# Performance work log

Measured on AMD Instinct MI355X. Metric: run time of the kernel, lower is better.

The kernel has to match this reference:

```python
import jax, jax.numpy as jnp
import numpy as np

B, S, D, H = 4, 2048, 1024, 16
DK = D // H

def setup_inputs() -> dict:
    key = jax.random.key(0)
    ks = jax.random.split(key, 8)
    scale = 1.0 / np.sqrt(D)
    q = jax.random.normal(ks[0], (B, S, D), dtype=jnp.float32)
    k = jax.random.normal(ks[1], (B, S, D), dtype=jnp.float32)
    v = jax.random.normal(ks[2], (B, S, D), dtype=jnp.float32)
    # Linear weights stored as [in, out] (applied as x @ W)
    W_q = jax.random.normal(ks[3], (D, D), dtype=jnp.float32) * scale
    W_k = jax.random.normal(ks[4], (D, D), dtype=jnp.float32) * scale
    W_v = jax.random.normal(ks[5], (D, D), dtype=jnp.float32) * scale
    W_o = jax.random.normal(ks[6], (D, D), dtype=jnp.float32) * scale
    mask = jnp.tril(jnp.ones((S, S), dtype=bool))[None, None]  # [1,1,S,S] causal
    return {"q": q, "k": k, "v": v, "W_q": W_q, "W_k": W_k, "W_v": W_v, "W_o": W_o, "mask": mask}

def reference(q, k, v, W_q, W_k, W_v, W_o, mask) -> jnp.ndarray:
    b, sq, _ = q.shape
    sk = k.shape[1]
    # project and split heads: [B,S,D] -> [B,H,S,dk]
    Q = (q @ W_q).reshape(b, sq, H, DK).transpose(0, 2, 1, 3)
    K = (k @ W_k).reshape(b, sk, H, DK).transpose(0, 2, 1, 3)
    V = (v @ W_v).reshape(b, sk, H, DK).transpose(0, 2, 1, 3)
    scores = jnp.einsum('bhqd,bhkd->bhqk', Q, K) / jnp.sqrt(jnp.float32(DK))
    scores = jnp.where(mask, scores, jnp.float32(-1e9))
    attn = jax.nn.softmax(scores, axis=-1)
    out = jnp.einsum('bhqk,bhkd->bhqd', attn, V)  # [B,H,Sq,dk]
    out = out.transpose(0, 2, 1, 3).reshape(b, sq, D)
    return out @ W_o
```

## Files before the change

kernel.cpp:

```cpp
#include <hip/hip_runtime.h>
#include <hip/hip_bf16.h>
#include <stdint.h>

#define B_  4
#define S_  2048
#define D_  1024
#define H_  16
#define DK_ 64
#define M_  (B_*S_)
#define MD_ ((size_t)M_*D_)

typedef unsigned short u16;
typedef unsigned int   u32;
using bh8 = __attribute__((ext_vector_type(8))) short;
using fx4 = __attribute__((ext_vector_type(4))) float;
using us4 = __attribute__((ext_vector_type(4))) unsigned short;

#define C1_ 0.18033688011112042f

__device__ __forceinline__ u16 f2bf(float f){
  union { float f; u32 u; } v; v.f = f;
  u32 r = v.u + 0x7FFFu + ((v.u >> 16) & 1u);
  return (u16)(r >> 16);
}
__device__ __forceinline__ u16 f2bf_fast(float f){
  union { float f; u32 u; } v; v.f = f;
  return (u16)((v.u + 0x8000u) >> 16);
}
__device__ __forceinline__ float fexp2(float x){
  float r;
  asm("v_exp_f32 %0, %1\n\ts_nop 0" : "=v"(r) : "v"(x));
  return r;
}
__device__ __forceinline__ void gl16(const void* g, void* l){
  __builtin_amdgcn_global_load_lds(
      (const __attribute__((address_space(1))) unsigned int*)g,
      (__attribute__((address_space(3))) unsigned int*)l, 16, 0, 0);
}

__global__ __launch_bounds__(256) void prep_k(const float* __restrict__ q,
                                              const float* __restrict__ k,
                                              const float* __restrict__ v,
                                              const float* __restrict__ W0,
                                              const float* __restrict__ W1,
                                              const float* __restrict__ W2,
                                              const float* __restrict__ W3,
                                              u16* __restrict__ dq,
                                              u16* __restrict__ dk,
                                              u16* __restrict__ dv,
                                              u16* __restrict__ WT){
  int id = blockIdx.x;
  int tid = threadIdx.x;
  if (id < 12288){
    int z = id >> 12;
    int i = (id & 4095)*256 + tid;
    const float* in = (z==0)? q : (z==1)? k : v;
    u16* out = (z==0)? dq : (z==1)? dk : dv;
    const float4* p = (const float4*)(in + (size_t)i*8);
    float4 a0 = p[0], a1 = p[1];
    u16 o[8];
    o[0]=f2bf(a0.x); o[1]=f2bf(a0.y); o[2]=f2bf(a0.z); o[3]=f2bf(a0.w);
    o[4]=f2bf(a1.x); o[5]=f2bf(a1.y); o[6]=f2bf(a1.z); o[7]=f2bf(a1.w);
    *(bh8*)(out + (size_t)i*8) = *(bh8*)o;
  } else {
    int id2 = id - 12288;
    int z = id2 >> 10, b2 = id2 & 1023;
    int bx = b2 & 31, by = b2 >> 5;
    const float* in = (z==0)? W0 : (z==1)? W1 : (z==2)? W2 : W3;
    float scale = (z==0)? C1_ : 1.0f;
    u16* o = WT + (size_t)z*1024*1024;
    __shared__ u16 tile[32][33];
    int tx = tid & 31, ty = tid >> 5;
    int x0 = bx*32, y0 = by*32;
    #pragma unroll
    for (int j=0;j<32;j+=8) tile[ty+j][tx] = f2bf(in[(size_t)(y0+ty+j)*D_ + x0+tx]*scale);
    __syncthreads();
    #pragma unroll
    for (int j=0;j<32;j+=8) o[(size_t)(x0+ty+j)*D_ + y0+tx] = tile[tx][ty+j];
  }
}

template<int MODE>
__global__ __launch_bounds__(512) void gemm8(const u16* __restrict__ Aqk,
                                             const u16* __restrict__ Av,
                                             const u16* __restrict__ WTb,
                                             u16* __restrict__ Cqk,
                                             u16* __restrict__ VtOut,
                                             float* __restrict__ Cf){
  __shared__ __align__(16) u16 AL[2][128*64];
  __shared__ __align__(16) u16 BL[2][256*64];

  int hbid = blockIdx.x;
  int xcd = hbid & 7, slot = hbid >> 3;
  int pg  = xcd * (MODE==0 ? 24 : 8) + (slot >> 2);
  int x   = slot & 3;
  int y   = (MODE==0) ? (pg & 63) : pg;
  int z   = (MODE==0) ? (pg >> 6) : 0;

  const u16* A  = (MODE==0 && z==2) ? Av : (Aqk + (size_t)z*MD_);
  const u16* BT = WTb + (size_t)z*1024*1024;
  int tid = threadIdx.x;
  int w = tid >> 6, lane = tid & 63, quad = lane >> 4, ln = lane & 15;
  int wm = w >> 2, wn = w & 3;
  int rowBase = y*128, colBase = x*256;

  auto sA = [&](int buf, int kt, int c){
    int s = c*512 + tid;
    int row = s >> 3, kc = (s & 7) ^ (row & 7);
    gl16(&A[(size_t)(rowBase + row)*D_ + kt*64 + kc*8], &AL[buf][s*8]);
  };
  auto sB = [&](int buf, int kt, int c){
    int s = c*512 + tid;
    int row = s >> 3, kc = (s & 7) ^ (row & 7);
    gl16(&BT[(size_t)(colBase + row)*D_ + kt*64 + kc*8], &BL[buf][s*8]);
  };
  auto ridx = [&](int row, int kc){ return row*64 + ((kc ^ (row & 7))*8); };

  fx4 acc[4][4];
  #pragma unroll
  for (int i=0;i<4;i++)
    #pragma unroll
    for (int j=0;j<4;j++) acc[i][j] = (fx4){0.f,0.f,0.f,0.f};

  sA(0,0,0); sA(0,0,1); sB(0,0,0); sB(0,0,1); sB(0,0,2); sB(0,0,3);
  sB(1,1,0); sB(1,1,1); sB(1,1,2);
  asm volatile("s_waitcnt vmcnt(3)" ::: "memory");
  __builtin_amdgcn_s_barrier();

  for (int it = 0; it < 8; ++it){
    int t = 2*it;
    bool h2 = (t+2 < 16), h3 = (t+3 < 16);
    #pragma unroll
    for (int half = 0; half < 2; ++half){
      const u16* Ab = &AL[half][0];
      const u16* Bb = &BL[half][0];

      bh8 bfr[4][2], af0[2][2], af1[2][2];
      #pragma unroll
      for (int n=0;n<4;n++)
        #pragma unroll
        for (int ks=0;ks<2;ks++)
          bfr[n][ks] = *(const bh8*)(&Bb[ridx(wn*64 + n*16 + ln, ks*4+quad)]);
      #pragma unroll
      for (int mi=0;mi<2;mi++)
        #pragma unroll
        for (int ks=0;ks<2;ks++)
          af0[mi][ks] = *(const bh8*)(&Ab[ridx(wm*64 + mi*16 + ln, ks*4+quad)]);
      #pragma unroll
      for (int mi=0;mi<2;mi++)
        #pragma unroll
        for (int ks=0;ks<2;ks++)
          af1[mi][ks] = *(const bh8*)(&Ab[ridx(wm*64 + 32 + mi*16 + ln, ks*4+quad)]);

      if (half == 0){
        sB(1, t+1, 3); sA(1, t+1, 0); sA(1, t+1, 1);
      } else if (h2){
        sB(0, t+2, 3); sA(0, t+2, 0); sA(0, t+2, 1);
      }
      __builtin_amdgcn_s_barrier();
      asm volatile("s_waitcnt lgkmcnt(4)" ::: "memory");
      __builtin_amdgcn_s_setprio(1);
      #pragma unroll
      for (int mi=0;mi<2;mi++)
        #pragma unroll
        for (int n=0;n<4;n++)
          #pragma unroll
          for (int ks=0;ks<2;ks++)
            acc[mi][n] = __builtin_amdgcn_mfma_f32_16x16x32_bf16(
                            af0[mi][ks], bfr[n][ks], acc[mi][n], 0,0,0);
      __builtin_amdgcn_s_setprio(0);
      __builtin_amdgcn_s_barrier();

      if (half == 0){
        if (h2){ sB(0, t+2, 0); sB(0, t+2, 1); sB(0, t+2, 2); }
        if (h2) asm volatile("s_waitcnt vmcnt(3)" ::: "memory");
        else    asm volatile("s_waitcnt vmcnt(0)" ::: "memory");
      } else {
        if (h3){ sB(1, t+3, 0); sB(1, t+3, 1); sB(1, t+3, 2); }
        if (h3) asm volatile("s_waitcnt vmcnt(3)" ::: "memory");
        else    asm volatile("s_waitcnt vmcnt(0)" ::: "memory");
      }
      __builtin_amdgcn_s_barrier();
      asm volatile("s_waitcnt lgkmcnt(0)" ::: "memory");
      __builtin_amdgcn_s_setprio(1);
      #pragma unroll
      for (int mi=0;mi<2;mi++)
        #pragma unroll
        for (int n=0;n<4;n++)
          #pragma unroll
          for (int ks=0;ks<2;ks++)
            acc[2+mi][n] = __builtin_amdgcn_mfma_f32_16x16x32_bf16(
                              af1[mi][ks], bfr[n][ks], acc[2+mi][n], 0,0,0);
      __builtin_amdgcn_s_setprio(0);
      __builtin_amdgcn_s_barrier();
    }
  }

  #pragma unroll
  for (int m=0;m<4;m++){
    int row0 = rowBase + wm*64 + m*16 + quad*4;
    #pragma unroll
    for (int n=0;n<4;n++){
      int col = colBase + wn*64 + n*16 + ln;
      if (MODE == 1){
        #pragma unroll
        for (int r=0;r<4;r++)
          Cf[(size_t)(row0 + r)*D_ + col] = acc[m][n][r];
      } else if (z == 2){
        int bb = row0 >> 11, tok = row0 & (S_-1);
        int hh = col >> 6,  vd  = col & 63;
        us4 pk;
        #pragma unroll
        for (int r=0;r<4;r++) pk[r] = f2bf(acc[m][n][r]);
        *(us4*)&VtOut[((size_t)((bb*16+hh)*64+vd))*S_ + tok] = pk;
      } else {
        #pragma unroll
        for (int r=0;r<4;r++)
          (Cqk + (size_t)z*MD_)[(size_t)(row0 + r)*D_ + col] = f2bf(acc[m][n][r]);
      }
    }
  }
}

__global__ __launch_bounds__(256) void attn_k(const u16* __restrict__ Q,
                                              const u16* __restrict__ Kp,
                                              const u16* __restrict__ VtG,
                                              u16* __restrict__ O){
  __shared__ __align__(16) u16 Kt[2][64*64];
  __shared__ __align__(16) u16 Vt[2][64*64];
  __shared__ __align__(16) u16 Pb[4*16*64];

  int bh = blockIdx.x; int b = bh>>4, h = bh&15;
  int qt = (int)gridDim.y - 1 - (int)blockIdx.y;
  int tid = threadIdx.x;
  int w = tid >> 6, lane = tid & 63, quad = lane >> 4, ln = lane & 15;
  int q0w = qt*128 + w*32;
  size_t headoff = (size_t)h*DK_;

  bh8 qf[2][2];
  #pragma unroll
  for (int rg=0; rg<2; rg++){
    const u16* qp = Q + (size_t)(b*S_ + q0w + rg*16 + ln)*D_ + headoff + quad*8;
    qf[rg][0] = *(const bh8*)qp;
    qf[rg][1] = *(const bh8*)(qp + 32);
  }

  float m_i[2], l_i[2];
  fx4 oacc[2][4];
  #pragma unroll
  for (int rg=0; rg<2; rg++){
    m_i[rg] = -3e38f; l_i[rg] = 0.f;
    #pragma unroll
    for (int r=0;r<4;r++) oacc[rg][r] = (fx4){0.f,0.f,0.f,0.f};
  }

  auto stage = [&](int k0, int bi){
    #pragma unroll
    for (int i=0;i<2;i++){
      int s = i*256 + tid;
      int n = s >> 3, kc = (s & 7) ^ (n & 7);
      gl16(&Kp[(size_t)(b*S_ + k0 + n)*D_ + headoff + kc*8], &Kt[bi][s*8]);
    }
    #pragma unroll
    for (int i=0;i<2;i++){
      int s = i*256 + tid;
      int vd = s >> 3, c = (s & 7) ^ (vd & 7);
      gl16(&VtG[(size_t)(bh*64 + vd)*S_ + k0 + c*8], &Vt[bi][s*8]);
    }
  };

  u16* Pw = &Pb[w*16*64];
  int ntiles = 2*qt + 2;

  stage(0, 0);
  __syncthreads();

  for (int kt=0; kt<ntiles; kt++){
    int cur = kt & 1;
    if (kt+1 < ntiles) stage((kt+1)*64, cur^1);
    const u16* Kc = Kt[cur];
    const u16* Vc = Vt[cur];
    int k0 = kt*64;
    bool diag = (kt >= 2*qt);

    #pragma unroll
    for (int rg=0; rg<2; rg++){
      fx4 sacc[4];
      __builtin_amdgcn_s_setprio(1);
      #pragma unroll
      for (int t=0;t<4;t++){
        int n = t*16 + ln;
        bh8 kf0 = *(const bh8*)(&Kc[(n*8 + ( quad    ^ (ln&7)))*8]);
        bh8 kf1 = *(const bh8*)(&Kc[(n*8 + ((4+quad) ^ (ln&7)))*8]);
        fx4 zz = (fx4){0.f,0.f,0.f,0.f};
        zz = __builtin_amdgcn_mfma_f32_16x16x32_bf16(kf0, qf[rg][0], zz, 0,0,0);
        zz = __builtin_amdgcn_mfma_f32_16x16x32_bf16(kf1, qf[rg][1], zz, 0,0,0);
        sacc[t] = zz;
      }
      __builtin_amdgcn_s_setprio(0);

      int qg = q0w + rg*16 + ln;
      if (diag){
        #pragma unroll
        for (int t=0;t<4;t++){
          #pragma unroll
          for (int r=0;r<4;r++){
            int kg = k0 + t*16 + quad*4 + r;
            sacc[t][r] = (kg <= qg) ? sacc[t][r] : -3e38f;
          }
        }
      }

      float tm[4];
      #pragma unroll
      for (int t=0;t<4;t++)
        tm[t] = fmaxf(fmaxf(sacc[t][0], sacc[t][1]), fmaxf(sacc[t][2], sacc[t][3]));
      float mloc = fmaxf(fmaxf(tm[0], tm[1]), fmaxf(tm[2], tm[3]));
      mloc = fmaxf(mloc, __shfl_xor(mloc, 16, 64));
      mloc = fmaxf(mloc, __shfl_xor(mloc, 32, 64));

      if (__any(mloc > m_i[rg] + 8.0f)){
        float mn = fmaxf(m_i[rg], mloc);
        float alpha = fexp2(m_i[rg] - mn);
        m_i[rg] = mn;
        l_i[rg] *= alpha;
        float al[4];
        #pragma unroll
        for (int r=0;r<4;r++) al[r] = __shfl(alpha, quad*4 + r, 64);
        #pragma unroll
        for (int vt=0;vt<4;vt++)
          #pragma unroll
          for (int r=0;r<4;r++)
            oacc[rg][vt][r] *= al[r];
      }
      float mn = m_i[rg];

      float ts[4];
      #pragma unroll
      for (int t=0;t<4;t++){
        #pragma unroll
        for (int r=0;r<4;r++) sacc[t][r] = fexp2(sacc[t][r] - mn);
        ts[t] = (sacc[t][0] + sacc[t][1]) + (sacc[t][2] + sacc[t][3]);
      }
      float rs = (ts[0] + ts[1]) + (ts[2] + ts[3]);
      rs += __shfl_xor(rs, 16, 64);
      rs += __shfl_xor(rs, 32, 64);
      l_i[rg] += rs;

      #pragma unroll
      for (int t=0;t<4;t++){
        int hs = (t*4 + quad) ^ (ln & 14);
        us4 pk;
        #pragma unroll
        for (int r=0;r<4;r++) pk[r] = f2bf_fast(sacc[t][r]);
        *(us4*)&Pw[ln*64 + hs*4] = pk;
      }
      asm volatile("s_waitcnt lgkmcnt(0)" ::: "memory");

      __builtin_amdgcn_s_setprio(1);
      #pragma unroll
      for (int s2=0; s2<2; s2++){
        int c = s2*4 + quad;
        int pm = c ^ ((ln>>1) & 7);
        bh8 pf = *(const bh8*)(&Pw[ln*64 + pm*8]);
        #pragma unroll
        for (int vt=0; vt<4; vt++){
          int vd = vt*16 + ln;
          bh8 vf = *(const bh8*)(&Vc[(vd*8 + (c ^ (ln&7)))*8]);
          oacc[rg][vt] = __builtin_amdgcn_mfma_f32_16x16x32_bf16(pf, vf, oacc[rg][vt], 0,0,0);
        }
      }
      __builtin_amdgcn_s_setprio(0);
      asm volatile("s_waitcnt lgkmcnt(0)" ::: "memory");
    }
    __syncthreads();
  }

  #pragma unroll
  for (int rg=0; rg<2; rg++){
    float linv = 1.0f / l_i[rg];
    float lb[4];
    #pragma unroll
    for (int r=0;r<4;r++) lb[r] = __shfl(linv, quad*4 + r, 64);
    #pragma unroll
    for (int r=0;r<4;r++){
      #pragma unroll
      for (int vt=0; vt<4; vt++){
        float ov = oacc[rg][vt][r] * lb[r];
        O[(size_t)(b*S_ + q0w + rg*16 + quad*4 + r)*D_ + headoff + vt*16 + ln] = f2bf(ov);
      }
    }
  }
}

extern "C" void kernel_launch(void* const* d_in, const int* in_sizes, int n_in,
                              void* d_out, int out_size, void* d_ws, size_t ws_size,
                              hipStream_t stream){
  const float* q  = (const float*)d_in[0];
  const float* k  = (const float*)d_in[1];
  const float* v  = (const float*)d_in[2];
  const float* Wq = (const float*)d_in[3];
  const float* Wk = (const float*)d_in[4];
  const float* Wv = (const float*)d_in[5];
  const float* Wo = (const float*)d_in[6];

  u16* ws  = (u16*)d_ws;
  u16* WT  = ws;
  u16* xa  = WT + (size_t)4*1024*1024;
  u16* xb  = xa + MD_;
  u16* Qp  = xb + MD_;
  u16* Kp  = Qp + MD_;

  u16* vb  = (u16*)d_out;
  u16* VtG = vb + MD_;

  prep_k<<<dim3(16384), 256, 0, stream>>>(q, k, v, Wq, Wk, Wv, Wo, xa, xb, vb, WT);

  gemm8<0><<<dim3(768), 512, 0, stream>>>(xa, vb, WT, Qp, VtG, nullptr);

  attn_k<<<dim3(B_*H_, S_/128), 256, 0, stream>>>(Qp, Kp, VtG, Qp);

  gemm8<1><<<dim3(256), 512, 0, stream>>>(Qp, nullptr, WT + (size_t)3*1024*1024,
                                          nullptr, nullptr, (float*)d_out);
}
```

Measured before the change: 326.5 us.

## Pair mirrored causal query tiles per block to balance attention work

Each attention block now handles two 64-row query tiles, j1=31-p and j2=p, back to back. This gives every block the same 33 KV tiles, replacing blocks of 128 query rows whose KV tile count grew with their position. Each wave now owns 16 query rows instead of 32, and the grid drops to 16 blocks per head on the y axis. The aim is to remove the causal load imbalance and tail effects, at the cost of each staged K/V tile feeding half as many query rows, which roughly doubles K/V staging traffic per query.

```diff
diff --git a/kernel.cpp b/kernel.cpp
--- a/kernel.cpp
+++ b/kernel.cpp
@@ -231,28 +231,40 @@
   __shared__ __align__(16) u16 Pb[4*16*64];
 
   int bh = blockIdx.x; int b = bh>>4, h = bh&15;
-  int qt = (int)gridDim.y - 1 - (int)blockIdx.y;
+  int p  = blockIdx.y;
+  int j1 = 31 - p, j2 = p;
   int tid = threadIdx.x;
   int w = tid >> 6, lane = tid & 63, quad = lane >> 4, ln = lane & 15;
-  int q0w = qt*128 + w*32;
   size_t headoff = (size_t)h*DK_;
 
-  bh8 qf[2][2];
-  #pragma unroll
-  for (int rg=0; rg<2; rg++){
-    const u16* qp = Q + (size_t)(b*S_ + q0w + rg*16 + ln)*D_ + headoff + quad*8;
-    qf[rg][0] = *(const bh8*)qp;
-    qf[rg][1] = *(const bh8*)(qp + 32);
-  }
-
-  float m_i[2], l_i[2];
-  fx4 oacc[2][4];
-  #pragma unroll
-  for (int rg=0; rg<2; rg++){
-    m_i[rg] = -3e38f; l_i[rg] = 0.f;
-    #pragma unroll
-    for (int r=0;r<4;r++) oacc[rg][r] = (fx4){0.f,0.f,0.f,0.f};
-  }
+  int q0w;
+  bh8 qf0, qf1;
+  float m_i, l_i;
+  fx4 oacc[4];
+
+  auto loadQ = [&](int j){
+    q0w = j*64 + w*16;
+    const u16* qp = Q + (size_t)(b*S_ + q0w + ln)*D_ + headoff + quad*8;
+    qf0 = *(const bh8*)qp;
+    qf1 = *(const bh8*)(qp + 32);
+    m_i = -3e38f; l_i = 0.f;
+    #pragma unroll
+    for (int r=0;r<4;r++) oacc[r] = (fx4){0.f,0.f,0.f,0.f};
+  };
+
+  auto writeO = [&](){
+    float linv = 1.0f / l_i;
+    float lb[4];
+    #pragma unroll
+    for (int r=0;r<4;r++) lb[r] = __shfl(linv, quad*4 + r, 64);
+    #pragma unroll
+    for (int r=0;r<4;r++)
+      #pragma unroll
+      for (int vt=0; vt<4; vt++){
+        float ov = oacc[vt][r] * lb[r];
+        O[(size_t)(b*S_ + q0w + quad*4 + r)*D_ + headoff + vt*16 + ln] = f2bf(ov);
+      }
+  };
 
   auto stage = [&](int k0, int bi){
     #pragma unroll
@@ -270,127 +282,116 @@
   };
 
   u16* Pw = &Pb[w*16*64];
-  int ntiles = 2*qt + 2;
-
+  const int nt = 33;
+  auto k0_of = [&](int i){ return (i <= j1) ? i*64 : (i - j1 - 1)*64; };
+
+  loadQ(j1);
   stage(0, 0);
   __syncthreads();
 
-  for (int kt=0; kt<ntiles; kt++){
-    int cur = kt & 1;
-    if (kt+1 < ntiles) stage((kt+1)*64, cur^1);
+  for (int i=0; i<nt; i++){
+    int cur = i & 1;
+    if (i+1 < nt) stage(k0_of(i+1), cur^1);
     const u16* Kc = Kt[cur];
     const u16* Vc = Vt[cur];
-    int k0 = kt*64;
-    bool diag = (kt >= 2*qt);
-
-    #pragma unroll
-    for (int rg=0; rg<2; rg++){
-      fx4 sacc[4];
-      __builtin_amdgcn_s_setprio(1);
-      #pragma unroll
-      for (int t=0;t<4;t++){
-        int n = t*16 + ln;
-        bh8 kf0 = *(const bh8*)(&Kc[(n*8 + ( quad    ^ (ln&7)))*8]);
-        bh8 kf1 = *(const bh8*)(&Kc[(n*8 + ((4+quad) ^ (ln&7)))*8]);
-        fx4 zz = (fx4){0.f,0.f,0.f,0.f};
-        zz = __builtin_amdgcn_mfma_f32_16x16x32_bf16(kf0, qf[rg][0], zz, 0,0,0);
-        zz = __builtin_amdgcn_mfma_f32_16x16x32_bf16(kf1, qf[rg][1], zz, 0,0,0);
-        sacc[t] = zz;
+    int k0 = k0_of(i);
+    bool diag = (i == j1) || (i == nt-1);
+
+    fx4 sacc[4];
+    __builtin_amdgcn_s_setprio(1);
+    #pragma unroll
+    for (int t=0;t<4;t++){
+      int n = t*16 + ln;
+      bh8 kf0 = *(const bh8*)(&Kc[(n*8 + ( quad    ^ (ln&7)))*8]);
+      bh8 kf1 = *(const bh8*)(&Kc[(n*8 + ((4+quad) ^ (ln&7)))*8]);
+      fx4 zz = (fx4){0.f,0.f,0.f,0.f};
+      zz = __builtin_amdgcn_mfma_f32_16x16x32_bf16(kf0, qf0, zz, 0,0,0);
+      zz = __builtin_amdgcn_mfma_f32_16x16x32_bf16(kf1, qf1, zz, 0,0,0);
+      sacc[t] = zz;
+    }
+    __builtin_amdgcn_s_setprio(0);
+
+    int qg = q0w + ln;
+    if (diag){
+      #pragma unroll
+      for (int t=0;t<4;t++)
+        #pragma unroll
+        for (int r=0;r<4;r++){
+          int kg = k0 + t*16 + quad*4 + r;
+          sacc[t][r] = (kg <= qg) ? sacc[t][r] : -3e38f;
+        }
+    }
+
+    float tm[4];
+    #pragma unroll
+    for (int t=0;t<4;t++)
+      tm[t] = fmaxf(fmaxf(sacc[t][0], sacc[t][1]), fmaxf(sacc[t][2], sacc[t][3]));
+    float mloc = fmaxf(fmaxf(tm[0], tm[1]), fmaxf(tm[2], tm[3]));
+    mloc = fmaxf(mloc, __shfl_xor(mloc, 16, 64));
+    mloc = fmaxf(mloc, __shfl_xor(mloc, 32, 64));
+
+    if (__any(mloc > m_i + 8.0f)){
+      float mn = fmaxf(m_i, mloc);
+      float alpha = fexp2(m_i - mn);
+      m_i = mn;
+      l_i *= alpha;
+      float al[4];
+      #pragma unroll
+      for (int r=0;r<4;r++) al[r] = __shfl(alpha, quad*4 + r, 64);
+      #pragma unroll
+      for (int vt=0;vt<4;vt++)
+        #pragma unroll
+        for (int r=0;r<4;r++)
+          oacc[vt][r] *= al[r];
+    }
+    float mn = m_i;
+
+    float ts[4];
+    #pragma unroll
+    for (int t=0;t<4;t++){
+      #pragma unroll
+      for (int r=0;r<4;r++) sacc[t][r] = fexp2(sacc[t][r] - mn);
+      ts[t] = (sacc[t][0] + sacc[t][1]) + (sacc[t][2] + sacc[t][3]);
+    }
+    float rs = (ts[0] + ts[1]) + (ts[2] + ts[3]);
+    rs += __shfl_xor(rs, 16, 64);
+    rs += __shfl_xor(rs, 32, 64);
+    l_i += rs;
+
+    #pragma unroll
+    for (int t=0;t<4;t++){
+      int hs = (t*4 + quad) ^ (ln & 14);
+      us4 pk;
+      #pragma unroll
+      for (int r=0;r<4;r++) pk[r] = f2bf_fast(sacc[t][r]);
+      *(us4*)&Pw[ln*64 + hs*4] = pk;
+    }
+    asm volatile("s_waitcnt lgkmcnt(0)" ::: "memory");
+
+    __builtin_amdgcn_s_setprio(1);
+    #pragma unroll
+    for (int s2=0; s2<2; s2++){
+      int c = s2*4 + quad;
+      int pm = c ^ ((ln>>1) & 7);
+      bh8 pf = *(const bh8*)(&Pw[ln*64 + pm*8]);
+      #pragma unroll
+      for (int vt=0; vt<4; vt++){
+        int vd = vt*16 + ln;
+        bh8 vf = *(const bh8*)(&Vc[(vd*8 + (c ^ (ln&7)))*8]);
+        oacc[vt] = __builtin_amdgcn_mfma_f32_16x16x32_bf16(pf, vf, oacc[vt], 0,0,0);
       }
-      __builtin_amdgcn_s_setprio(0);
-
-      int qg = q0w + rg*16 + ln;
-      if (diag){
-        #pragma unroll
-        for (int t=0;t<4;t++){
-          #pragma unroll
-          for (int r=0;r<4;r++){
-            int kg = k0 + t*16 + quad*4 + r;
-            sacc[t][r] = (kg <= qg) ? sacc[t][r] : -3e38f;
-          }
-        }
-      }
-
-      float tm[4];
-      #pragma unroll
-      for (int t=0;t<4;t++)
-        tm[t] = fmaxf(fmaxf(sacc[t][0], sacc[t][1]), fmaxf(sacc[t][2], sacc[t][3]));
-      float mloc = fmaxf(fmaxf(tm[0], tm[1]), fmaxf(tm[2], tm[3]));
-      mloc = fmaxf(mloc, __shfl_xor(mloc, 16, 64));
-      mloc = fmaxf(mloc, __shfl_xor(mloc, 32, 64));
-
-      if (__any(mloc > m_i[rg] + 8.0f)){
-        float mn = fmaxf(m_i[rg], mloc);
-        float alpha = fexp2(m_i[rg] - mn);
-        m_i[rg] = mn;
-        l_i[rg] *= alpha;
-        float al[4];
-        #pragma unroll
-        for (int r=0;r<4;r++) al[r] = __shfl(alpha, quad*4 + r, 64);
-        #pragma unroll
-        for (int vt=0;vt<4;vt++)
-          #pragma unroll
-          for (int r=0;r<4;r++)
-            oacc[rg][vt][r] *= al[r];
-      }
-      float mn = m_i[rg];
-
-      float ts[4];
-      #pragma unroll
-      for (int t=0;t<4;t++){
-        #pragma unroll
-        for (int r=0;r<4;r++) sacc[t][r] = fexp2(sacc[t][r] - mn);
-        ts[t] = (sacc[t][0] + sacc[t][1]) + (sacc[t][2] + sacc[t][3]);
-      }
-      float rs = (ts[0] + ts[1]) + (ts[2] + ts[3]);
-      rs += __shfl_xor(rs, 16, 64);
-      rs += __shfl_xor(rs, 32, 64);
-      l_i[rg] += rs;
-
-      #pragma unroll
-      for (int t=0;t<4;t++){
-        int hs = (t*4 + quad) ^ (ln & 14);
-        us4 pk;
-        #pragma unroll
-        for (int r=0;r<4;r++) pk[r] = f2bf_fast(sacc[t][r]);
-        *(us4*)&Pw[ln*64 + hs*4] = pk;
-      }
-      asm volatile("s_waitcnt lgkmcnt(0)" ::: "memory");
-
-      __builtin_amdgcn_s_setprio(1);
-      #pragma unroll
-      for (int s2=0; s2<2; s2++){
-        int c = s2*4 + quad;
-        int pm = c ^ ((ln>>1) & 7);
-        bh8 pf = *(const bh8*)(&Pw[ln*64 + pm*8]);
-        #pragma unroll
-        for (int vt=0; vt<4; vt++){
-          int vd = vt*16 + ln;
-          bh8 vf = *(const bh8*)(&Vc[(vd*8 + (c ^ (ln&7)))*8]);
-          oacc[rg][vt] = __builtin_amdgcn_mfma_f32_16x16x32_bf16(pf, vf, oacc[rg][vt], 0,0,0);
-        }
-      }
-      __builtin_amdgcn_s_setprio(0);
-      asm volatile("s_waitcnt lgkmcnt(0)" ::: "memory");
+    }
+    __builtin_amdgcn_s_setprio(0);
+    asm volatile("s_waitcnt lgkmcnt(0)" ::: "memory");
+
+    if (i == j1){
+      writeO();
+      loadQ(j2);
     }
     __syncthreads();
   }
 
-  #pragma unroll
-  for (int rg=0; rg<2; rg++){
-    float linv = 1.0f / l_i[rg];
-    float lb[4];
-    #pragma unroll
-    for (int r=0;r<4;r++) lb[r] = __shfl(linv, quad*4 + r, 64);
-    #pragma unroll
-    for (int r=0;r<4;r++){
-      #pragma unroll
-      for (int vt=0; vt<4; vt++){
-        float ov = oacc[rg][vt][r] * lb[r];
-        O[(size_t)(b*S_ + q0w + rg*16 + quad*4 + r)*D_ + headoff + vt*16 + ln] = f2bf(ov);
-      }
-    }
-  }
+  writeO();
 }
 
 extern "C" void kernel_launch(void* const* d_in, const int* in_sizes, int n_in,
@@ -418,7 +419,7 @@
 
   gemm8<0><<<dim3(768), 512, 0, stream>>>(xa, vb, WT, Qp, VtG, nullptr);
 
-  attn_k<<<dim3(B_*H_, S_/128), 256, 0, stream>>>(Qp, Kp, VtG, Qp);
+  attn_k<<<dim3(B_*H_, 16), 256, 0, stream>>>(Qp, Kp, VtG, Qp);
 
   gemm8<1><<<dim3(256), 512, 0, stream>>>(Qp, nullptr, WT + (size_t)3*1024*1024,
                                           nullptr, nullptr, (float*)d_out);
```

After: 319.9 us. 1.02x faster.
